# Optimization experiments

Measured on AMD Instinct MI355X. Metric: run time of the kernel, lower is better.

## Reference

```python
import jax, jax.numpy as jnp
import numpy as np

N_NODES = 50000
N_EDGES = 800000
D_IN = 96
HID = 128


def _glorot(key, shape):
    fan_in, fan_out = shape[0], shape[1]
    lim = np.sqrt(6.0 / (fan_in + fan_out)).astype(np.float32)
    return jax.random.uniform(key, shape, jnp.float32, -lim, lim)


def setup_inputs() -> dict:
    key = jax.random.key(0)
    ks = jax.random.split(key, 12)
    x = jax.random.normal(ks[0], (N_NODES, D_IN), jnp.float32)
    edge_index = jax.random.randint(ks[1], (2, N_EDGES), 0, N_NODES)
    return {
        "x": x,
        "edge_index": edge_index,
        "W_in": _glorot(ks[2], (D_IN, HID)),
        "b_in": jnp.zeros((HID,), jnp.float32),
        "W1": _glorot(ks[3], (HID, HID)),
        "b1": jnp.zeros((HID,), jnp.float32),
        "W2": _glorot(ks[4], (HID, HID)),
        "b2": jnp.zeros((HID,), jnp.float32),
        "Wm1": _glorot(ks[5], (2 * HID, HID)),
        "bm1": jnp.zeros((HID,), jnp.float32),
        "Wm2": _glorot(ks[6], (HID, 1)),
        "bm2": jnp.zeros((1,), jnp.float32),
    }


def _gcn_conv(h, W, b, src, dst, n_nodes):
    # PyG GCNConv with add_self_loops=True, normalize=True:
    # out = D^{-1/2} (A + I) D^{-1/2} (h W) + b, aggregating x_j (source) into dst.
    loop = jnp.arange(n_nodes)
    row = jnp.concatenate([src, loop])  # source / j
    col = jnp.concatenate([dst, loop])  # target / i
    deg = jax.ops.segment_sum(jnp.ones(row.shape, h.dtype), col, num_segments=n_nodes)
    dinv = jnp.where(deg > 0, jax.lax.rsqrt(deg), 0.0)
    norm = dinv[row] * dinv[col]  # [E+N]
    xw = h @ W  # [N, H]
    msg = xw[row] * norm[:, None]  # gather + scale, [E+N, H]
    out = jax.ops.segment_sum(msg, col, num_segments=n_nodes)  # scatter-add
    return out + b


def reference(x, edge_index, W_in, b_in, W1, b1, W2, b2, Wm1, bm1, Wm2, bm2):
    src, dst = edge_index[0], edge_index[1]
    n = x.shape[0]
    h = jax.nn.relu(x @ W_in + b_in)  # dropout is identity at inference
    h = jax.nn.relu(_gcn_conv(h, W1, b1, src, dst, n))
    h = jax.nn.relu(_gcn_conv(h, W2, b2, src, dst, n))
    ef = jnp.concatenate([h[src], h[dst]], axis=1)  # [E, 2H]
    hid = jax.nn.relu(ef @ Wm1 + bm1)
    logits = (hid @ Wm2 + bm2)[:, 0]  # [E]
    return logits
```

## Files before the change

### kernel.cpp

```cpp
#include <hip/hip_runtime.h>

#define N_NODES 50000
#define N_EDGES 800000
#define D_IN 96
#define HID 128
#define NB 391
#define BCAP 3072
#define ECAP 1024

typedef __attribute__((ext_vector_type(8))) _Float16 halfx8;
typedef __attribute__((ext_vector_type(4))) _Float16 half4v;
typedef __attribute__((ext_vector_type(2))) _Float16 half2v;
typedef __attribute__((ext_vector_type(16))) float f32x16;

__device__ inline float dot2acc(half2v a, half2v b, float c) {
#if __has_builtin(__builtin_amdgcn_fdot2)
    return __builtin_amdgcn_fdot2(a, b, c, false);
#else
    return c + (float)a[0] * (float)b[0] + (float)a[1] * (float)b[1];
#endif
}

__device__ inline halfx8 relu8(halfx8 s) {
#if __has_builtin(__builtin_elementwise_max)
    return __builtin_elementwise_max(s, (halfx8)0);
#else
    halfx8 r;
#pragma unroll
    for (int i = 0; i < 8; i++) r[i] = s[i] > (_Float16)0 ? s[i] : (_Float16)0;
    return r;
#endif
}

__global__ __launch_bounds__(256) void hist_pack_kernel(const int* __restrict__ dst,
                                                        int* __restrict__ bhist,
                                                        const float* __restrict__ W_in,
                                                        const float* __restrict__ W1,
                                                        const float* __restrict__ W2,
                                                        const float* __restrict__ Wm1,
                                                        const float* __restrict__ Wm2,
                                                        _Float16* __restrict__ packed) {
    __shared__ int lh[NB];
    int t = threadIdx.x;
    if (blockIdx.x < 196) {
        for (int i = t; i < NB; i += 256) lh[i] = 0;
        __syncthreads();
        int base = blockIdx.x * 4096;
#pragma unroll
        for (int i = 0; i < 16; i++) {
            int e = base + i * 256 + t;
            if (e < N_EDGES) atomicAdd(&lh[dst[e] >> 7], 1);
        }
        __syncthreads();
        for (int i = t; i < NB; i += 256) atomicAdd(&bhist[i], lh[i]);
        return;
    }
    int g = (blockIdx.x - 196) * 256 + t;
    if (g >= 77952) return;
    if (g >= 77824) { packed[g] = (_Float16)Wm2[g - 77824]; return; }
    const float* Wsrc;
    int K, u;
    if (g < 12288)      { Wsrc = W_in;            K = 96;  u = g; }
    else if (g < 28672) { Wsrc = W1;              K = 128; u = g - 12288; }
    else if (g < 45056) { Wsrc = W2;              K = 128; u = g - 28672; }
    else if (g < 61440) { Wsrc = Wm1;             K = 128; u = g - 45056; }
    else                { Wsrc = Wm1 + 128 * 128; K = 128; u = g - 61440; }
    int steps = K >> 4;
    int cb = u / (steps * 512);
    int rem = u - cb * steps * 512;
    int s = rem >> 9;
    int lane = (rem >> 3) & 63;
    int j = rem & 7;
    int k = s * 16 + ((lane >> 5) << 3) + j;
    int n = (cb << 5) + (lane & 31);
    packed[g] = (_Float16)Wsrc[k * 128 + n];
}

__global__ __launch_bounds__(512) void scan_buckets_kernel(const int* __restrict__ bhist,
                                                           int* __restrict__ boff,
                                                           int* __restrict__ bcursor) {
    __shared__ int s[512];
    int t = threadIdx.x;
    int v = (t < NB) ? bhist[t] : 0;
    s[t] = v;
    __syncthreads();
    for (int off = 1; off < 512; off <<= 1) {
        int u = (t >= off) ? s[t - off] : 0;
        __syncthreads();
        s[t] += u;
        __syncthreads();
    }
    if (t < NB) {
        int ex = s[t] - v;
        boff[t] = ex;
        bcursor[t] = ex;
    }
    if (t == NB - 1) boff[NB] = s[t];
}

__global__ __launch_bounds__(512) void bin_kernel(const int* __restrict__ src,
                                                  const int* __restrict__ dst,
                                                  int* __restrict__ bcursor,
                                                  unsigned long long* __restrict__ binned) {
    __shared__ int lh[NB];
    __shared__ int gbs[NB];
    int t = threadIdx.x;
    for (int i = t; i < NB; i += 512) lh[i] = 0;
    __syncthreads();
    int base = blockIdx.x * 8192;
    unsigned long long pk[16];
    int bb[16], rk[16];
#pragma unroll
    for (int i = 0; i < 16; i++) {
        int e = base + i * 512 + t;
        bb[i] = -1;
        if (e < N_EDGES) {
            int s = src[e], d = dst[e];
            int b = d >> 7;
            bb[i] = b;
            pk[i] = ((unsigned long long)s << 27) |
                    ((unsigned long long)(d & 127) << 20) | (unsigned long long)e;
            rk[i] = atomicAdd(&lh[b], 1);
        }
    }
    __syncthreads();
    for (int i = t; i < NB; i += 512) gbs[i] = atomicAdd(&bcursor[i], lh[i]);
    __syncthreads();
#pragma unroll
    for (int i = 0; i < 16; i++) {
        if (bb[i] >= 0) binned[gbs[bb[i]] + rk[i]] = pk[i];
    }
}

__global__ __launch_bounds__(256) void bucket_sort_kernel(const unsigned long long* __restrict__ binned,
                                                          const int* __restrict__ boff,
                                                          int* __restrict__ ce_src,
                                                          int* __restrict__ ce_eid,
                                                          int* __restrict__ ce_dst,
                                                          int* __restrict__ csr_ptr,
                                                          float* __restrict__ dinv) {
    __shared__ int2 sorted[BCAP];
    __shared__ int cntA[128], sc[128];
    int b = blockIdx.x;
    int t = threadIdx.x;
    int base = boff[b];
    int k = boff[b + 1] - base;
    if (k > BCAP) k = BCAP;
    if (t < 128) cntA[t] = 0;
    __syncthreads();
    unsigned long long pk[12];
    int rk[12];
#pragma unroll
    for (int m = 0; m < 12; m++) {
        int i = t + m * 256;
        rk[m] = -1;
        if (i < k) {
            unsigned long long p = binned[base + i];
            pk[m] = p;
            int d = (int)((p >> 20) & 127);
            rk[m] = atomicAdd(&cntA[d], 1);
        }
    }
    __syncthreads();
    if (t < 128) sc[t] = cntA[t];
    __syncthreads();
    for (int off = 1; off < 128; off <<= 1) {
        int u = 0;
        if (t < 128 && t >= off) u = sc[t - off];
        __syncthreads();
        if (t < 128) sc[t] += u;
        __syncthreads();
    }
#pragma unroll
    for (int m = 0; m < 12; m++) {
        if (rk[m] >= 0) {
            unsigned long long p = pk[m];
            int d = (int)((p >> 20) & 127);
            int pos = sc[d] - cntA[d] + rk[m];
            int srcn = (int)(p >> 27);
            int eid = (int)(p & 0xFFFFF);
            sorted[pos] = make_int2(srcn | (d << 16), eid);
        }
    }
    __syncthreads();
    for (int i = t; i < k; i += 256) {
        int2 se = sorted[i];
        ce_src[base + i] = se.x & 0xFFFF;
        ce_eid[base + i] = se.y;
        ce_dst[base + i] = (b << 7) + (se.x >> 16);
    }
    if (t < 128) {
        int node = (b << 7) + t;
        if (node < N_NODES) {
            csr_ptr[node] = base + sc[t] - cntA[t];
            dinv[node] = 1.0f / sqrtf((float)(cntA[t] + 1));
        }
    }
    if (b == NB - 1 && t == 0) csr_ptr[N_NODES] = boff[NB];
}

__global__ __launch_bounds__(256) void fused_in_kernel(const float* __restrict__ x,
                                                       const _Float16* __restrict__ WpIn,
                                                       const _Float16* __restrict__ Wp1,
                                                       const float* __restrict__ b_in,
                                                       const float* __restrict__ dinv,
                                                       _Float16* __restrict__ y1, int M) {
    __shared__ _Float16 As[32 * 104];
    __shared__ _Float16 Hs[32 * 136];
    int tid = threadIdx.x;
    int M0 = blockIdx.x * 32;
    for (int i = tid; i < 32 * 24; i += 256) {
        int r = i / 24, c = i - r * 24;
        float4 v = make_float4(0.f, 0.f, 0.f, 0.f);
        int row = M0 + r;
        if (row < M) v = *(const float4*)&x[(size_t)row * 96 + c * 4];
        half2v a = {(_Float16)v.x, (_Float16)v.y};
        half2v b = {(_Float16)v.z, (_Float16)v.w};
        *(half2v*)&As[r * 104 + c * 4] = a;
        *(half2v*)&As[r * 104 + c * 4 + 2] = b;
    }
    __syncthreads();

    int wave = tid >> 6, lane = tid & 63;
    int col = wave * 32 + (lane & 31);
    {
        const halfx8* bp = (const halfx8*)WpIn + (size_t)wave * 6 * 64 + lane;
        const _Float16* arow = &As[(lane & 31) * 104 + ((lane >> 5) << 3)];
        f32x16 acc = {};
#pragma unroll
        for (int s = 0; s < 6; s++) {
            halfx8 a = *(const halfx8*)&arow[s * 16];
            acc = __builtin_amdgcn_mfma_f32_32x32x16_f16(a, bp[s * 64], acc, 0, 0, 0);
        }
        float bA = b_in[col];
#pragma unroll
        for (int r = 0; r < 16; r++) {
            int rl = (r & 3) + 8 * (r >> 2) + 4 * (lane >> 5);
            Hs[rl * 136 + col] = (_Float16)fmaxf(acc[r] + bA, 0.f);
        }
    }
    __syncthreads();
    {
        const halfx8* bp = (const halfx8*)Wp1 + (size_t)wave * 8 * 64 + lane;
        const _Float16* arow = &Hs[(lane & 31) * 136 + ((lane >> 5) << 3)];
        f32x16 acc = {};
#pragma unroll
        for (int s = 0; s < 8; s++) {
            halfx8 a = *(const halfx8*)&arow[s * 16];
            acc = __builtin_amdgcn_mfma_f32_32x32x16_f16(a, bp[s * 64], acc, 0, 0, 0);
        }
#pragma unroll
        for (int r = 0; r < 16; r++) {
            int rl = (r & 3) + 8 * (r >> 2) + 4 * (lane >> 5);
            int grow = M0 + rl;
            if (grow < M) {
                y1[(size_t)grow * 128 + col] = (_Float16)(acc[r] * dinv[grow]);
            }
        }
    }
}

__global__ __launch_bounds__(256) void gemm_f16_kernel(const _Float16* __restrict__ A,
                                                       const _Float16* __restrict__ Wp,
                                                       const float* __restrict__ bias,
                                                       const float* __restrict__ rowscale,
                                                       _Float16* __restrict__ out,
                                                       int M, int K, int steps, int dorelu) {
    __shared__ _Float16 As[32 * 136];
    int tid = threadIdx.x;
    int M0 = blockIdx.x * 32;
    int stride = K + 8;
    int CH = K >> 3;
    int tot = 32 * CH;
    for (int i = tid; i < tot; i += 256) {
        int r = i / CH, c = i - r * CH;
        uint4 v = make_uint4(0, 0, 0, 0);
        int row = M0 + r;
        if (row < M) v = *(const uint4*)&A[(size_t)row * K + c * 8];
        *(uint4*)&As[r * stride + c * 8] = v;
    }
    __syncthreads();

    int wave = tid >> 6, lane = tid & 63;
    const halfx8* bp = (const halfx8*)Wp + (size_t)wave * steps * 64 + lane;
    const _Float16* arow = &As[(lane & 31) * stride + ((lane >> 5) << 3)];
    f32x16 acc = {};
    for (int s = 0; s < steps; s++) {
        halfx8 a = *(const halfx8*)&arow[s * 16];
        acc = __builtin_amdgcn_mfma_f32_32x32x16_f16(a, bp[s * 64], acc, 0, 0, 0);
    }
    int col = wave * 32 + (lane & 31);
    float bA = bias ? bias[col] : 0.f;
#pragma unroll
    for (int r = 0; r < 16; r++) {
        int rl = (r & 3) + 8 * (r >> 2) + 4 * (lane >> 5);
        int grow = M0 + rl;
        if (grow < M) {
            float sc = rowscale ? rowscale[grow] : 1.f;
            float v0 = (acc[r] + bA) * sc;
            if (dorelu) v0 = fmaxf(v0, 0.f);
            out[(size_t)grow * 128 + col] = (_Float16)v0;
        }
    }
}

__global__ __launch_bounds__(256) void gemm_uv_kernel(const _Float16* __restrict__ A,
                                                      const _Float16* __restrict__ WpU,
                                                      const _Float16* __restrict__ WpV,
                                                      const float* __restrict__ bm1,
                                                      _Float16* __restrict__ U,
                                                      _Float16* __restrict__ V,
                                                      int M) {
    const int K = 128, steps = 8;
    __shared__ _Float16 As[32 * 136];
    int tid = threadIdx.x;
    int M0 = blockIdx.x * 32;
    int stride = K + 8;
    for (int i = tid; i < 32 * 16; i += 256) {
        int r = i >> 4, c = i & 15;
        uint4 v = make_uint4(0, 0, 0, 0);
        int row = M0 + r;
        if (row < M) v = *(const uint4*)&A[(size_t)row * K + c * 8];
        *(uint4*)&As[r * stride + c * 8] = v;
    }
    __syncthreads();

    int wave = tid >> 6, lane = tid & 63;
    const halfx8* bu = (const halfx8*)WpU + (size_t)wave * steps * 64 + lane;
    const halfx8* bv = (const halfx8*)WpV + (size_t)wave * steps * 64 + lane;
    const _Float16* arow = &As[(lane & 31) * stride + ((lane >> 5) << 3)];
    f32x16 au = {}, av = {};
#pragma unroll
    for (int s = 0; s < steps; s++) {
        halfx8 a = *(const halfx8*)&arow[s * 16];
        au = __builtin_amdgcn_mfma_f32_32x32x16_f16(a, bu[s * 64], au, 0, 0, 0);
        av = __builtin_amdgcn_mfma_f32_32x32x16_f16(a, bv[s * 64], av, 0, 0, 0);
    }
    int col = wave * 32 + (lane & 31);
    float bA = bm1[col];
#pragma unroll
    for (int r = 0; r < 16; r++) {
        int rl = (r & 3) + 8 * (r >> 2) + 4 * (lane >> 5);
        int grow = M0 + rl;
        if (grow < M) {
            U[(size_t)grow * 128 + col] = (_Float16)(au[r] + bA);
            V[(size_t)grow * 128 + col] = (_Float16)av[r];
        }
    }
}

__global__ __launch_bounds__(256, 6) void aggregate_kernel(const _Float16* __restrict__ y,
                                                           const float* __restrict__ dinv,
                                                           const int* __restrict__ ptr,
                                                           const int* __restrict__ ce_src,
                                                           const float* __restrict__ bias,
                                                           _Float16* __restrict__ out) {
    __shared__ int sidx[ECAP];
    __shared__ int sptr[9];
    int node0 = blockIdx.x * 8;
    int tid = threadIdx.x;
    if (tid < 9) sptr[tid] = ptr[node0 + tid];
    __syncthreads();
    int base = sptr[0];
    int tot = sptr[8] - base;
    bool fit = (tot <= ECAP);
    if (fit) {
        for (int i = tid; i < tot; i += 256) sidx[i] = ce_src[base + i];
    }
    __syncthreads();

    int hw = tid >> 5;
    int l = tid & 31;
    int node = node0 + hw;
    float di = dinv[node];
    half4v self = ((const half4v*)&y[(size_t)node * 128])[l];
    float a0 = (float)self[0], a1 = (float)self[1], a2 = (float)self[2], a3 = (float)self[3];
    float b0 = 0.f, b1 = 0.f, b2 = 0.f, b3 = 0.f;
    int s0 = sptr[hw], s1 = sptr[hw + 1];

    if (fit) {
        int j = s0 - base, e = s1 - base;
        while (j < e) {
            half4v v[16];
#pragma unroll
            for (int k = 0; k < 16; k++) {
                int idx = j + k;
                int n = sidx[idx < e ? idx : e - 1];
                v[k] = ((const half4v*)&y[(size_t)n * 128])[l];
            }
            __builtin_amdgcn_sched_barrier(0);
#pragma unroll
            for (int k = 0; k < 16; k += 2) {
                float m0 = (j + k < e) ? 1.f : 0.f;
                float m1 = (j + k + 1 < e) ? 1.f : 0.f;
                a0 += m0 * (float)v[k][0];     a1 += m0 * (float)v[k][1];
                a2 += m0 * (float)v[k][2];     a3 += m0 * (float)v[k][3];
                b0 += m1 * (float)v[k + 1][0]; b1 += m1 * (float)v[k + 1][1];
                b2 += m1 * (float)v[k + 1][2]; b3 += m1 * (float)v[k + 1][3];
            }
            j += 16;
        }
    } else {
        for (int j = s0; j < s1; j++) {
            int n = ce_src[j];
            half4v v = ((const half4v*)&y[(size_t)n * 128])[l];
            a0 += (float)v[0]; a1 += (float)v[1]; a2 += (float)v[2]; a3 += (float)v[3];
        }
    }
    float4 bv = *(const float4*)&bias[l * 4];
    half4v ov;
    ov[0] = (_Float16)fmaxf(di * (a0 + b0) + bv.x, 0.f);
    ov[1] = (_Float16)fmaxf(di * (a1 + b1) + bv.y, 0.f);
    ov[2] = (_Float16)fmaxf(di * (a2 + b2) + bv.z, 0.f);
    ov[3] = (_Float16)fmaxf(di * (a3 + b3) + bv.w, 0.f);
    ((half4v*)&out[(size_t)node * 128])[l] = ov;
}

__global__ __launch_bounds__(256) void edge_mlp_kernel(const _Float16* __restrict__ Ub,
                                                       const _Float16* __restrict__ Vb,
                                                       const int* __restrict__ ce_src,
                                                       const int* __restrict__ ce_eid,
                                                       const int* __restrict__ ce_dst,
                                                       const _Float16* __restrict__ Wm2h,
                                                       const float* __restrict__ bm2,
                                                       float* __restrict__ out) {
    __shared__ int ssrc[128], sdst[128], seid[128];
    int tid = threadIdx.x;
    int e0 = blockIdx.x * 128;
    if (tid < 128) {
        ssrc[tid] = ce_src[e0 + tid];
        seid[tid] = ce_eid[e0 + tid];
    } else {
        sdst[tid - 128] = ce_dst[e0 + tid - 128];
    }
    __syncthreads();
    int g = tid >> 4;
    int l = tid & 15;
    halfx8 wv = *(const halfx8*)&Wm2h[l * 8];
    half2v w0 = {wv[0], wv[1]}, w1 = {wv[2], wv[3]}, w2 = {wv[4], wv[5]}, w3 = {wv[6], wv[7]};
    halfx8 uu[8], vv[8];
#pragma unroll
    for (int k = 0; k < 8; k++) {
        int e = g + 16 * k;
        uu[k] = *(const halfx8*)&Ub[(size_t)ssrc[e] * 128 + l * 8];
        vv[k] = *(const halfx8*)&Vb[(size_t)sdst[e] * 128 + l * 8];
    }
    __builtin_amdgcn_sched_barrier(0);
    float p[8];
#pragma unroll
    for (int k = 0; k < 8; k++) {
        halfx8 s = relu8(uu[k] + vv[k]);
        half2v s0 = {s[0], s[1]}, s1 = {s[2], s[3]}, s2 = {s[4], s[5]}, s3 = {s[6], s[7]};
        float acc = dot2acc(s0, w0, 0.f);
        acc = dot2acc(s1, w1, acc);
        acc = dot2acc(s2, w2, acc);
        p[k] = dot2acc(s3, w3, acc);
    }
#pragma unroll
    for (int d = 1; d < 16; d <<= 1) {
#pragma unroll
        for (int k = 0; k < 8; k++) p[k] += __shfl_xor(p[k], d);
    }
    if (l == 0) {
        float bb = bm2[0];
#pragma unroll
        for (int k = 0; k < 8; k++) out[seid[g + 16 * k]] = p[k] + bb;
    }
}

extern "C" void kernel_launch(void* const* d_in, const int* in_sizes, int n_in,
                              void* d_out, int out_size, void* d_ws, size_t ws_size,
                              hipStream_t stream) {
    const float* x    = (const float*)d_in[0];
    const int* eidx   = (const int*)d_in[1];
    const float* W_in = (const float*)d_in[2];
    const float* b_in = (const float*)d_in[3];
    const float* W1   = (const float*)d_in[4];
    const float* b1   = (const float*)d_in[5];
    const float* W2   = (const float*)d_in[6];
    const float* b2   = (const float*)d_in[7];
    const float* Wm1  = (const float*)d_in[8];
    const float* bm1  = (const float*)d_in[9];
    const float* Wm2  = (const float*)d_in[10];
    const float* bm2  = (const float*)d_in[11];
    float* out = (float*)d_out;
    const int* src = eidx;
    const int* dst = eidx + N_EDGES;

    char* w = (char*)d_ws;
    size_t off = 0;
    auto alloc = [&](size_t bytes) -> char* {
        char* p = w + off;
        off = (off + bytes + 255) & ~(size_t)255;
        return p;
    };
    int* bhist    = (int*)alloc((size_t)NB * 4);
    int* boff     = (int*)alloc((size_t)(NB + 1) * 4);
    int* bcursor  = (int*)alloc((size_t)NB * 4);
    int* csr_ptr  = (int*)alloc((size_t)(N_NODES + 1) * 4);
    float* dinv   = (float*)alloc((size_t)N_NODES * 4);
    unsigned long long* binned = (unsigned long long*)alloc((size_t)N_EDGES * 8);
    int* ce_src   = (int*)alloc((size_t)N_EDGES * 4);
    int* ce_eid   = (int*)alloc((size_t)N_EDGES * 4);
    int* ce_dst   = (int*)alloc((size_t)N_EDGES * 4);
    _Float16* Wp  = (_Float16*)alloc((size_t)77952 * 2);
    _Float16* y1  = (_Float16*)alloc((size_t)N_NODES * HID * 2);
    _Float16* y2  = (_Float16*)alloc((size_t)N_NODES * HID * 2);
    _Float16* hbuf = (_Float16*)alloc((size_t)N_NODES * HID * 2);
    _Float16* Ub  = (_Float16*)alloc((size_t)N_NODES * HID * 2);
    _Float16* Vb  = (_Float16*)alloc((size_t)N_NODES * HID * 2);

    const _Float16* WpIn  = Wp;
    const _Float16* Wp1   = Wp + 12288;
    const _Float16* Wp2   = Wp + 28672;
    const _Float16* WpM1a = Wp + 45056;
    const _Float16* WpM1b = Wp + 61440;
    const _Float16* Wm2h  = Wp + 77824;

    hipMemsetAsync(bhist, 0, (size_t)NB * 4, stream);
    hist_pack_kernel<<<196 + 305, 256, 0, stream>>>(dst, bhist, W_in, W1, W2, Wm1, Wm2, Wp);
    scan_buckets_kernel<<<1, 512, 0, stream>>>(bhist, boff, bcursor);
    bin_kernel<<<98, 512, 0, stream>>>(src, dst, bcursor, binned);
    bucket_sort_kernel<<<NB, 256, 0, stream>>>(binned, boff, ce_src, ce_eid, ce_dst,
                                               csr_ptr, dinv);

    int gblocks = (N_NODES + 31) / 32;
    fused_in_kernel<<<gblocks, 256, 0, stream>>>(x, WpIn, Wp1, b_in, dinv, y1, N_NODES);
    aggregate_kernel<<<N_NODES / 8, 256, 0, stream>>>(y1, dinv, csr_ptr, ce_src, b1, hbuf);
    gemm_f16_kernel<<<gblocks, 256, 0, stream>>>(hbuf, Wp2, nullptr, dinv, y2,
                                                 N_NODES, HID, 8, 0);
    aggregate_kernel<<<N_NODES / 8, 256, 0, stream>>>(y2, dinv, csr_ptr, ce_src, b2, hbuf);
    gemm_uv_kernel<<<gblocks, 256, 0, stream>>>(hbuf, WpM1a, WpM1b, bm1, Ub, Vb, N_NODES);
    edge_mlp_kernel<<<N_EDGES / 128, 256, 0, stream>>>(Ub, Vb, ce_src, ce_eid, ce_dst,
                                                       Wm2h, bm2, out);
}
```

Before: 256.5 us.

## Split node features into four 32-column slices to localize aggregation gathers

Node feature buffers change from row-major [N,128] to four column-slice planes of [N,32]. Producer GEMMs write this sliced layout and consumer GEMMs read from it. The aggregation kernel now handles 16 nodes per block for one slice, with block indices interleaved so that concurrently scheduled blocks share a slice. The aim is to shrink the working set of the random neighbor gathers to a quarter of the feature table, so gathers hit in L2/MALL more often. In exchange, each block handles a narrower half2 load per lane and the edge index list is read four times.

```diff
diff --git a/kernel.cpp b/kernel.cpp
--- a/kernel.cpp
+++ b/kernel.cpp
@@ -6,7 +6,7 @@
 #define HID 128
 #define NB 391
 #define BCAP 3072
-#define ECAP 1024
+#define AECAP 768
 
 typedef __attribute__((ext_vector_type(8))) _Float16 halfx8;
 typedef __attribute__((ext_vector_type(4))) _Float16 half4v;
@@ -254,7 +254,8 @@
             int rl = (r & 3) + 8 * (r >> 2) + 4 * (lane >> 5);
             int grow = M0 + rl;
             if (grow < M) {
-                y1[(size_t)grow * 128 + col] = (_Float16)(acc[r] * dinv[grow]);
+                y1[((size_t)wave * N_NODES + grow) * 32 + (lane & 31)] =
+                    (_Float16)(acc[r] * dinv[grow]);
             }
         }
     }
@@ -265,18 +266,18 @@
                                                        const float* __restrict__ bias,
                                                        const float* __restrict__ rowscale,
                                                        _Float16* __restrict__ out,
-                                                       int M, int K, int steps, int dorelu) {
+                                                       int M, int steps, int dorelu) {
+    const int K = 128;
     __shared__ _Float16 As[32 * 136];
     int tid = threadIdx.x;
     int M0 = blockIdx.x * 32;
     int stride = K + 8;
-    int CH = K >> 3;
-    int tot = 32 * CH;
-    for (int i = tid; i < tot; i += 256) {
-        int r = i / CH, c = i - r * CH;
+    for (int i = tid; i < 32 * 16; i += 256) {
+        int r = i >> 4, c = i & 15;
         uint4 v = make_uint4(0, 0, 0, 0);
         int row = M0 + r;
-        if (row < M) v = *(const uint4*)&A[(size_t)row * K + c * 8];
+        if (row < M)
+            v = *(const uint4*)&A[((size_t)(c >> 2) * N_NODES + row) * 32 + (c & 3) * 8];
         *(uint4*)&As[r * stride + c * 8] = v;
     }
     __syncthreads();
@@ -299,7 +300,7 @@
             float sc = rowscale ? rowscale[grow] : 1.f;
             float v0 = (acc[r] + bA) * sc;
             if (dorelu) v0 = fmaxf(v0, 0.f);
-            out[(size_t)grow * 128 + col] = (_Float16)v0;
+            out[((size_t)wave * N_NODES + grow) * 32 + (lane & 31)] = (_Float16)v0;
         }
     }
 }
@@ -320,7 +321,8 @@
         int r = i >> 4, c = i & 15;
         uint4 v = make_uint4(0, 0, 0, 0);
         int row = M0 + r;
-        if (row < M) v = *(const uint4*)&A[(size_t)row * K + c * 8];
+        if (row < M)
+            v = *(const uint4*)&A[((size_t)(c >> 2) * N_NODES + row) * 32 + (c & 3) * 8];
         *(uint4*)&As[r * stride + c * 8] = v;
     }
     __syncthreads();
@@ -355,38 +357,43 @@
                                                            const int* __restrict__ ce_src,
                                                            const float* __restrict__ bias,
                                                            _Float16* __restrict__ out) {
-    __shared__ int sidx[ECAP];
-    __shared__ int sptr[9];
-    int node0 = blockIdx.x * 8;
+    __shared__ int sidx[AECAP];
+    __shared__ int sptr[17];
+    int b = blockIdx.x;
+    int sl = (b & 7) >> 1;
+    int o = ((b >> 3) << 1) + (b & 1);
+    if (o >= 3125) return;
+    int node0 = o * 16;
     int tid = threadIdx.x;
-    if (tid < 9) sptr[tid] = ptr[node0 + tid];
+    if (tid < 17) sptr[tid] = ptr[node0 + tid];
     __syncthreads();
     int base = sptr[0];
-    int tot = sptr[8] - base;
-    bool fit = (tot <= ECAP);
+    int tot = sptr[16] - base;
+    bool fit = (tot <= AECAP);
     if (fit) {
         for (int i = tid; i < tot; i += 256) sidx[i] = ce_src[base + i];
     }
     __syncthreads();
 
-    int hw = tid >> 5;
-    int l = tid & 31;
-    int node = node0 + hw;
+    int g = tid >> 4;
+    int l = tid & 15;
+    int node = node0 + g;
     float di = dinv[node];
-    half4v self = ((const half4v*)&y[(size_t)node * 128])[l];
-    float a0 = (float)self[0], a1 = (float)self[1], a2 = (float)self[2], a3 = (float)self[3];
-    float b0 = 0.f, b1 = 0.f, b2 = 0.f, b3 = 0.f;
-    int s0 = sptr[hw], s1 = sptr[hw + 1];
+    const _Float16* ys = y + (size_t)sl * N_NODES * 32 + l * 2;
+    half2v self = *(const half2v*)&ys[(size_t)node * 32];
+    float a0 = (float)self[0], a1 = (float)self[1];
+    float b0 = 0.f, b1 = 0.f;
+    int s0 = sptr[g], s1 = sptr[g + 1];
 
     if (fit) {
         int j = s0 - base, e = s1 - base;
         while (j < e) {
-            half4v v[16];
+            half2v v[16];
 #pragma unroll
             for (int k = 0; k < 16; k++) {
                 int idx = j + k;
                 int n = sidx[idx < e ? idx : e - 1];
-                v[k] = ((const half4v*)&y[(size_t)n * 128])[l];
+                v[k] = *(const half2v*)&ys[(size_t)n * 32];
             }
             __builtin_amdgcn_sched_barrier(0);
 #pragma unroll
@@ -394,26 +401,22 @@
                 float m0 = (j + k < e) ? 1.f : 0.f;
                 float m1 = (j + k + 1 < e) ? 1.f : 0.f;
                 a0 += m0 * (float)v[k][0];     a1 += m0 * (float)v[k][1];
-                a2 += m0 * (float)v[k][2];     a3 += m0 * (float)v[k][3];
                 b0 += m1 * (float)v[k + 1][0]; b1 += m1 * (float)v[k + 1][1];
-                b2 += m1 * (float)v[k + 1][2]; b3 += m1 * (float)v[k + 1][3];
             }
             j += 16;
         }
     } else {
         for (int j = s0; j < s1; j++) {
             int n = ce_src[j];
-            half4v v = ((const half4v*)&y[(size_t)n * 128])[l];
-            a0 += (float)v[0]; a1 += (float)v[1]; a2 += (float)v[2]; a3 += (float)v[3];
-        }
-    }
-    float4 bv = *(const float4*)&bias[l * 4];
-    half4v ov;
+            half2v v = *(const half2v*)&ys[(size_t)n * 32];
+            a0 += (float)v[0]; a1 += (float)v[1];
+        }
+    }
+    float2 bv = *(const float2*)&bias[sl * 32 + l * 2];
+    half2v ov;
     ov[0] = (_Float16)fmaxf(di * (a0 + b0) + bv.x, 0.f);
     ov[1] = (_Float16)fmaxf(di * (a1 + b1) + bv.y, 0.f);
-    ov[2] = (_Float16)fmaxf(di * (a2 + b2) + bv.z, 0.f);
-    ov[3] = (_Float16)fmaxf(di * (a3 + b3) + bv.w, 0.f);
-    ((half4v*)&out[(size_t)node * 128])[l] = ov;
+    *(half2v*)&out[((size_t)sl * N_NODES + node) * 32 + l * 2] = ov;
 }
 
 __global__ __launch_bounds__(256) void edge_mlp_kernel(const _Float16* __restrict__ Ub,
@@ -525,11 +528,12 @@
                                                csr_ptr, dinv);
 
     int gblocks = (N_NODES + 31) / 32;
+    int ablocks = 1563 * 8;
     fused_in_kernel<<<gblocks, 256, 0, stream>>>(x, WpIn, Wp1, b_in, dinv, y1, N_NODES);
-    aggregate_kernel<<<N_NODES / 8, 256, 0, stream>>>(y1, dinv, csr_ptr, ce_src, b1, hbuf);
+    aggregate_kernel<<<ablocks, 256, 0, stream>>>(y1, dinv, csr_ptr, ce_src, b1, hbuf);
     gemm_f16_kernel<<<gblocks, 256, 0, stream>>>(hbuf, Wp2, nullptr, dinv, y2,
-                                                 N_NODES, HID, 8, 0);
-    aggregate_kernel<<<N_NODES / 8, 256, 0, stream>>>(y2, dinv, csr_ptr, ce_src, b2, hbuf);
+                                                 N_NODES, 8, 0);
+    aggregate_kernel<<<ablocks, 256, 0, stream>>>(y2, dinv, csr_ptr, ce_src, b2, hbuf);
     gemm_uv_kernel<<<gblocks, 256, 0, stream>>>(hbuf, WpM1a, WpM1b, bm1, Ub, Vb, N_NODES);
     edge_mlp_kernel<<<N_EDGES / 128, 256, 0, stream>>>(Ub, Vb, ce_src, ce_eid, ce_dst,
                                                        Wm2h, bm2, out);
```

Measured after the change: 269.8 us. 5.2% more time.
